# Kernel optimization log

Hardware: AMD Instinct MI355X
Metric: run time of the kernel (lower is better)

Reference implementation:

```python
import jax, jax.numpy as jnp
import numpy as np

B, N, E, H = 16, 512, 512, 8
D = E // H
NEG = -1e9  # stands in for -inf; other scores are clamped to [-10, 10]


def setup_inputs() -> dict:
    key = jax.random.key(0)
    ks = jax.random.split(key, 11)
    s = 1.0 / np.sqrt(E)
    return {
        "x": jax.random.normal(ks[0], (B, N, E), jnp.float32),
        "db": jax.random.normal(ks[1], (B, N, N), jnp.float32),
        "mask": jax.random.randint(ks[2], (B, N), 0, 2, jnp.int32),
        "wq": jax.random.normal(ks[3], (E, E), jnp.float32) * s,
        "bq": jax.random.normal(ks[4], (E,), jnp.float32) * s,
        "wk": jax.random.normal(ks[5], (E, E), jnp.float32) * s,
        "bk": jax.random.normal(ks[6], (E,), jnp.float32) * s,
        "wv": jax.random.normal(ks[7], (E, E), jnp.float32) * s,
        "bv": jax.random.normal(ks[8], (E,), jnp.float32) * s,
        "wo": jax.random.normal(ks[9], (E, E), jnp.float32) * s,
        "bo": jax.random.normal(ks[10], (E,), jnp.float32) * s,
    }


def reference(x, db, mask, wq, bq, wk, bk, wv, bv, wo, bo):
    # projections -> [B, H, N, D]
    def proj(w, b):
        return (x @ w.T + b).reshape(B, N, H, D).transpose(0, 2, 1, 3)

    q = proj(wq, bq)
    k = proj(wk, bk)
    v = proj(wv, bv)

    scale = 1.0 / np.sqrt(D).astype(np.float32)
    sc = jnp.einsum('bhid,bhjd->bhij', q, k) * scale + db[:, None, :, :]
    sc = jnp.clip(sc, -10.0, 10.0)
    sc = jnp.where(mask[:, None, None, :].astype(bool), sc, NEG)
    a = jax.nn.softmax(sc, axis=-1)  # dropout is identity (p=0 / eval)
    o = jnp.einsum('bhij,bhjd->bhid', a, v)
    o = o.transpose(0, 2, 1, 3).reshape(B, N, E)
    return o @ wo.T + bo
```

## Files before the change

### kernel.cpp

```cpp
#include <hip/hip_runtime.h>

typedef __attribute__((ext_vector_type(8))) short short8;
typedef __attribute__((ext_vector_type(4))) short short4v;
typedef __attribute__((ext_vector_type(4))) float f32x4;

#define MFMA16(A, B, C) __builtin_amdgcn_mfma_f32_16x16x32_bf16(A, B, C, 0, 0, 0)

__device__ __forceinline__ short f2bf(float f) {
    union { float f; unsigned u; } v;
    v.f = f;
    unsigned r = (v.u + 0x7FFFu + ((v.u >> 16) & 1u)) >> 16;
    return (short)r;
}

__device__ __forceinline__ float bf2f(short u) {
    union { unsigned u; float f; } v;
    v.u = ((unsigned)(unsigned short)u) << 16;
    return v.f;
}

__global__ __launch_bounds__(256) void cvt_all(
    const float* __restrict__ x, const float* __restrict__ wq,
    const float* __restrict__ wk, const float* __restrict__ wv,
    const float* __restrict__ wo, const float* __restrict__ db,
    const int* __restrict__ mask, short* __restrict__ xb,
    short* __restrict__ wcat, short* __restrict__ wob,
    short* __restrict__ dbp) {
    const int blk = blockIdx.x;
    if (blk < 2560) {
        int i = blk * 256 + threadIdx.x;
        const float* src;
        short* dst;
        int soff, doff;
        if (i < 524288) {
            src = x; dst = xb; soff = i; doff = i;
        } else {
            int j = i - 524288;
            int w = j >> 15;
            soff = j & 32767;
            src = (w == 0) ? wq : (w == 1) ? wk : (w == 2) ? wv : wo;
            if (w < 3) { dst = wcat; doff = j; }
            else       { dst = wob;  doff = soff; }
        }
        const float* p = src + (size_t)soff * 8;
        short8 r;
#pragma unroll
        for (int t = 0; t < 8; ++t) r[t] = f2bf(p[t]);
        *(short8*)(dst + (size_t)doff * 8) = r;
    } else {
        int t = (blk - 2560) * 256 + threadIdx.x;
        int f = t * 8;
        int b = f >> 18;
        int rem = f & 262143;
        int qt = rem >> 13;
        int rem2 = rem & 8191;
        int jidx = rem2 >> 10;
        int w = rem2 & 1023;
        int lane = w >> 4;
        int idx0 = w & 15;
        int c = lane & 15, g = lane >> 4;
        int q = qt * 16 + c;
        const float* dbrow = db + ((size_t)b * 512 + q) * 512;
        const int* mrow = mask + b * 512;
        short8 out;
#pragma unroll
        for (int e = 0; e < 8; ++e) {
            int idx = idx0 + e;
            int nt = idx >> 2, r = idx & 3;
            int j = jidx * 64 + nt * 16 + g * 4 + r;
            float val = (mrow[j] != 0) ? dbrow[j] : -1e9f;
            out[e] = f2bf(val);
        }
        *(short8*)(dbp + (size_t)f) = out;
    }
}

__global__ __launch_bounds__(256) void qkv128(
    const short* __restrict__ A, const short* __restrict__ Bw,
    const float* __restrict__ bq, const float* __restrict__ bk,
    const float* __restrict__ bv, short* __restrict__ qo,
    short* __restrict__ ko, short* __restrict__ vto) {
    __shared__ short As[128 * 72];
    __shared__ short Bs[128 * 72];
    const int tid = threadIdx.x, lane = tid & 63, wid = tid >> 6;
    const int c = lane & 15, g = lane >> 4;
    const int wr = (wid >> 1) * 64, wc = (wid & 1) * 64;
    const int m0 = blockIdx.x * 128, e0 = blockIdx.y * 128;

    const f32x4 Z = {0.f, 0.f, 0.f, 0.f};
    f32x4 acc[4][4];
#pragma unroll
    for (int i = 0; i < 4; ++i)
#pragma unroll
        for (int j = 0; j < 4; ++j) acc[i][j] = Z;

    short8 pa[4], pb[4];
#pragma unroll
    for (int p = 0; p < 4; ++p) {
        int u = p * 256 + tid;
        int row = u >> 3, c8 = u & 7;
        pa[p] = *(const short8*)&A[(size_t)(m0 + row) * 512 + c8 * 8];
        pb[p] = *(const short8*)&Bw[(size_t)(e0 + row) * 512 + c8 * 8];
    }
    for (int it = 0; it < 8; ++it) {
        __syncthreads();
#pragma unroll
        for (int p = 0; p < 4; ++p) {
            int u = p * 256 + tid;
            int row = u >> 3, c8 = u & 7;
            *(short8*)&As[row * 72 + c8 * 8] = pa[p];
            *(short8*)&Bs[row * 72 + c8 * 8] = pb[p];
        }
        if (it < 7) {
            int k0 = (it + 1) * 64;
#pragma unroll
            for (int p = 0; p < 4; ++p) {
                int u = p * 256 + tid;
                int row = u >> 3, c8 = u & 7;
                pa[p] = *(const short8*)&A[(size_t)(m0 + row) * 512 + k0 + c8 * 8];
                pb[p] = *(const short8*)&Bw[(size_t)(e0 + row) * 512 + k0 + c8 * 8];
            }
        }
        __syncthreads();
#pragma unroll
        for (int ks = 0; ks < 2; ++ks) {
            short8 af[4], bf[4];
#pragma unroll
            for (int mt = 0; mt < 4; ++mt)
                af[mt] = *(const short8*)&As[(wr + mt * 16 + c) * 72 + ks * 32 + g * 8];
#pragma unroll
            for (int nt = 0; nt < 4; ++nt)
                bf[nt] = *(const short8*)&Bs[(wc + nt * 16 + c) * 72 + ks * 32 + g * 8];
#pragma unroll
            for (int mt = 0; mt < 4; ++mt)
#pragma unroll
                for (int nt = 0; nt < 4; ++nt)
                    acc[mt][nt] = MFMA16(af[mt], bf[nt], acc[mt][nt]);
        }
    }

    const int z = e0 >> 9;
    const float* bp = (z == 0) ? bq : (z == 1) ? bk : bv;
    if (z < 2) {
        short* out = (z == 0) ? qo : ko;
#pragma unroll
        for (int nt = 0; nt < 4; ++nt) {
            int eh = (e0 & 511) + wc + nt * 16 + c;
            float bsv = bp[eh];
            int h = eh >> 6, d = eh & 63;
#pragma unroll
            for (int mt = 0; mt < 4; ++mt)
#pragma unroll
                for (int r = 0; r < 4; ++r) {
                    int m = m0 + wr + mt * 16 + g * 4 + r;
                    int bb = m >> 9, n = m & 511;
                    out[(((size_t)bb * 8 + h) * 512 + n) * 64 + d] =
                        f2bf(acc[mt][nt][r] + bsv);
                }
        }
    } else {
#pragma unroll
        for (int nt = 0; nt < 4; ++nt) {
            int eh = (e0 & 511) + wc + nt * 16 + c;
            float bsv = bp[eh];
            int h = eh >> 6, d = eh & 63;
#pragma unroll
            for (int mt = 0; mt < 4; ++mt) {
                int m = m0 + wr + mt * 16 + g * 4;
                int bb = m >> 9, n = m & 511;
                short4v w;
#pragma unroll
                for (int r = 0; r < 4; ++r) w[r] = f2bf(acc[mt][nt][r] + bsv);
                *(short4v*)&vto[(((size_t)bb * 8 + h) * 64 + d) * 512 + n] = w;
            }
        }
    }
}

__global__ __launch_bounds__(256) void out128(const short* __restrict__ A,
                                              const short* __restrict__ W,
                                              const float* __restrict__ bo,
                                              float* __restrict__ out) {
    __shared__ short As[128 * 72];
    __shared__ short Bs[128 * 72];
    const int tid = threadIdx.x, lane = tid & 63, wid = tid >> 6;
    const int c = lane & 15, g = lane >> 4;
    const int wr = (wid >> 1) * 64, wc = (wid & 1) * 64;
    const int m0 = blockIdx.x * 128, e0 = blockIdx.y * 128;

    const f32x4 Z = {0.f, 0.f, 0.f, 0.f};
    f32x4 acc[4][4];
#pragma unroll
    for (int i = 0; i < 4; ++i)
#pragma unroll
        for (int j = 0; j < 4; ++j) acc[i][j] = Z;

    short8 pa[4], pb[4];
#pragma unroll
    for (int p = 0; p < 4; ++p) {
        int u = p * 256 + tid;
        int row = u >> 3, c8 = u & 7;
        pa[p] = *(const short8*)&A[(size_t)(m0 + row) * 512 + c8 * 8];
        pb[p] = *(const short8*)&W[(size_t)(e0 + row) * 512 + c8 * 8];
    }
    for (int it = 0; it < 8; ++it) {
        __syncthreads();
#pragma unroll
        for (int p = 0; p < 4; ++p) {
            int u = p * 256 + tid;
            int row = u >> 3, c8 = u & 7;
            *(short8*)&As[row * 72 + c8 * 8] = pa[p];
            *(short8*)&Bs[row * 72 + c8 * 8] = pb[p];
        }
        if (it < 7) {
            int k0 = (it + 1) * 64;
#pragma unroll
            for (int p = 0; p < 4; ++p) {
                int u = p * 256 + tid;
                int row = u >> 3, c8 = u & 7;
                pa[p] = *(const short8*)&A[(size_t)(m0 + row) * 512 + k0 + c8 * 8];
                pb[p] = *(const short8*)&W[(size_t)(e0 + row) * 512 + k0 + c8 * 8];
            }
        }
        __syncthreads();
#pragma unroll
        for (int ks = 0; ks < 2; ++ks) {
            short8 af[4], bf[4];
#pragma unroll
            for (int mt = 0; mt < 4; ++mt)
                af[mt] = *(const short8*)&As[(wr + mt * 16 + c) * 72 + ks * 32 + g * 8];
#pragma unroll
            for (int nt = 0; nt < 4; ++nt)
                bf[nt] = *(const short8*)&Bs[(wc + nt * 16 + c) * 72 + ks * 32 + g * 8];
#pragma unroll
            for (int mt = 0; mt < 4; ++mt)
#pragma unroll
                for (int nt = 0; nt < 4; ++nt)
                    acc[mt][nt] = MFMA16(af[mt], bf[nt], acc[mt][nt]);
        }
    }

#pragma unroll
    for (int nt = 0; nt < 4; ++nt) {
        int e = e0 + wc + nt * 16 + c;
        float bsv = bo[e];
#pragma unroll
        for (int mt = 0; mt < 4; ++mt)
#pragma unroll
            for (int r = 0; r < 4; ++r) {
                int m = m0 + wr + mt * 16 + g * 4 + r;
                out[(size_t)m * 512 + e] = acc[mt][nt][r] + bsv;
            }
    }
}

__global__ __launch_bounds__(256, 2) void attn_mfma(
    const short* __restrict__ q, const short* __restrict__ k,
    const short* __restrict__ vt, const short* __restrict__ dbp_all,
    short* __restrict__ o) {
    __shared__ short pl[8][16 * 72];
    const int tid = threadIdx.x;
    const int lane = tid & 63, wid = tid >> 6;
    const int c = lane & 15, g = lane >> 4;
    const int f = blockIdx.x;
    const int blo = f & 7;
    const int t = f >> 3;
    const int u4 = t & 3;
    const int h = (t >> 2) & 7;
    const int b = (t >> 5) * 8 + blo;
    const int u = u4 * 4 + wid;
    const int q0A = u * 32;

    const short* kp = k + (((size_t)b * 8 + h) * 512) * 64;
    const short* vp = vt + (((size_t)b * 8 + h) * 64) * 512;
    const short* qpA = q + (((size_t)b * 8 + h) * 512 + q0A) * 64;
    const short* dbpA = dbp_all + (((size_t)b * 32 + u * 2) * 8) * 1024 + lane * 16;
    const short* dbpB = dbpA + 8192;

    short8 qA0 = *(const short8*)&qpA[c * 64 + g * 8];
    short8 qA1 = *(const short8*)&qpA[c * 64 + 32 + g * 8];
    short8 qB0 = *(const short8*)&qpA[(16 + c) * 64 + g * 8];
    short8 qB1 = *(const short8*)&qpA[(16 + c) * 64 + 32 + g * 8];

    short8 kf0[4], kf1[4];
#pragma unroll
    for (int nt = 0; nt < 4; ++nt) {
        kf0[nt] = *(const short8*)&kp[(nt * 16 + c) * 64 + g * 8];
        kf1[nt] = *(const short8*)&kp[(nt * 16 + c) * 64 + 32 + g * 8];
    }
    short8 dA0 = *(const short8*)&dbpA[0];
    short8 dA1 = *(const short8*)&dbpA[8];
    short8 dB0 = *(const short8*)&dbpB[0];
    short8 dB1 = *(const short8*)&dbpB[8];

    const f32x4 Z = {0.f, 0.f, 0.f, 0.f};
    f32x4 oA[4], oB[4];
    float lsA[4], lsB[4];
#pragma unroll
    for (int dt = 0; dt < 4; ++dt) { oA[dt] = Z; oB[dt] = Z; }
#pragma unroll
    for (int nt = 0; nt < 4; ++nt) { lsA[nt] = 0.f; lsB[nt] = 0.f; }

    short* plA = &pl[wid * 2][0];
    short* plB = &pl[wid * 2 + 1][0];

    for (int jidx = 0; jidx < 8; ++jidx) {
        const int j0 = jidx * 64;
        f32x4 sA[4], sB[4];
        __builtin_amdgcn_s_setprio(1);
#pragma unroll
        for (int nt = 0; nt < 4; ++nt) {
            f32x4 zA = Z, zB = Z;
            zA = MFMA16(kf0[nt], qA0, zA);
            zB = MFMA16(kf0[nt], qB0, zB);
            zA = MFMA16(kf1[nt], qA1, zA);
            zB = MFMA16(kf1[nt], qB1, zB);
            sA[nt] = zA;
            sB[nt] = zB;
        }
        __builtin_amdgcn_s_setprio(0);
        if (jidx < 7) {
#pragma unroll
            for (int nt = 0; nt < 4; ++nt) {
                kf0[nt] = *(const short8*)&kp[(j0 + 64 + nt * 16 + c) * 64 + g * 8];
                kf1[nt] = *(const short8*)&kp[(j0 + 64 + nt * 16 + c) * 64 + 32 + g * 8];
            }
        }
        short8 vf0[4], vf1[4];
#pragma unroll
        for (int dt = 0; dt < 4; ++dt) {
            vf0[dt] = *(const short8*)&vp[(dt * 16 + c) * 512 + j0 + g * 8];
            vf1[dt] = *(const short8*)&vp[(dt * 16 + c) * 512 + j0 + 32 + g * 8];
        }
#pragma unroll
        for (int nt = 0; nt < 4; ++nt) {
            short4v w;
            float ps0 = 0.f, ps1 = 0.f;
#pragma unroll
            for (int r = 0; r < 4; ++r) {
                int idx = nt * 4 + r;
                float dv = bf2f(idx < 8 ? dA0[idx] : dA1[idx - 8]);
                float v = fminf(fmaxf(fmaf(sA[nt][r], 0.125f, dv), -10.f), 10.f);
                float pp = exp2f(fmaf(v, 1.442695041f, -14.42695041f));
                w[r] = f2bf(pp);
                if (r < 2) ps0 += pp; else ps1 += pp;
            }
            lsA[nt] += ps0 + ps1;
            *(short4v*)&plA[c * 72 + nt * 16 + g * 4] = w;
        }
        if (jidx < 7) {
            dA0 = *(const short8*)&dbpA[(jidx + 1) * 1024];
            dA1 = *(const short8*)&dbpA[(jidx + 1) * 1024 + 8];
        }
#pragma unroll
        for (int nt = 0; nt < 4; ++nt) {
            short4v w;
            float ps0 = 0.f, ps1 = 0.f;
#pragma unroll
            for (int r = 0; r < 4; ++r) {
                int idx = nt * 4 + r;
                float dv = bf2f(idx < 8 ? dB0[idx] : dB1[idx - 8]);
                float v = fminf(fmaxf(fmaf(sB[nt][r], 0.125f, dv), -10.f), 10.f);
                float pp = exp2f(fmaf(v, 1.442695041f, -14.42695041f));
                w[r] = f2bf(pp);
                if (r < 2) ps0 += pp; else ps1 += pp;
            }
            lsB[nt] += ps0 + ps1;
            *(short4v*)&plB[c * 72 + nt * 16 + g * 4] = w;
        }
        if (jidx < 7) {
            dB0 = *(const short8*)&dbpB[(jidx + 1) * 1024];
            dB1 = *(const short8*)&dbpB[(jidx + 1) * 1024 + 8];
        }
        asm volatile("s_waitcnt lgkmcnt(0)" ::: "memory");
        __builtin_amdgcn_sched_barrier(0);
        short8 pA0 = *(const short8*)&plA[c * 72 + g * 8];
        short8 pA1 = *(const short8*)&plA[c * 72 + 32 + g * 8];
        short8 pB0 = *(const short8*)&plB[c * 72 + g * 8];
        short8 pB1 = *(const short8*)&plB[c * 72 + 32 + g * 8];
        __builtin_amdgcn_s_setprio(1);
#pragma unroll
        for (int dt = 0; dt < 4; ++dt) {
            oA[dt] = MFMA16(vf0[dt], pA0, oA[dt]);
            oB[dt] = MFMA16(vf0[dt], pB0, oB[dt]);
            oA[dt] = MFMA16(vf1[dt], pA1, oA[dt]);
            oB[dt] = MFMA16(vf1[dt], pB1, oB[dt]);
        }
        __builtin_amdgcn_s_setprio(0);
    }
    float lA = (lsA[0] + lsA[1]) + (lsA[2] + lsA[3]);
    lA += __shfl_xor(lA, 16);
    lA += __shfl_xor(lA, 32);
    float lB = (lsB[0] + lsB[1]) + (lsB[2] + lsB[3]);
    lB += __shfl_xor(lB, 16);
    lB += __shfl_xor(lB, 32);
    const float invA = 1.f / lA, invB = 1.f / lB;
#pragma unroll
    for (int dt = 0; dt < 4; ++dt) {
        short4v wa, wb;
#pragma unroll
        for (int r = 0; r < 4; ++r) {
            wa[r] = f2bf(oA[dt][r] * invA);
            wb[r] = f2bf(oB[dt][r] * invB);
        }
        *(short4v*)&o[((size_t)b * 512 + q0A + c) * 512 + h * 64 + dt * 16 + g * 4] = wa;
        *(short4v*)&o[((size_t)b * 512 + q0A + 16 + c) * 512 + h * 64 + dt * 16 + g * 4] = wb;
    }
}

extern "C" void kernel_launch(void* const* d_in, const int* in_sizes, int n_in,
                              void* d_out, int out_size, void* d_ws, size_t ws_size,
                              hipStream_t stream) {
    const float* x  = (const float*)d_in[0];
    const float* db = (const float*)d_in[1];
    const int* msk  = (const int*)d_in[2];
    const float* wq = (const float*)d_in[3];
    const float* bq = (const float*)d_in[4];
    const float* wk = (const float*)d_in[5];
    const float* bk = (const float*)d_in[6];
    const float* wv = (const float*)d_in[7];
    const float* bv = (const float*)d_in[8];
    const float* wo = (const float*)d_in[9];
    const float* bo = (const float*)d_in[10];
    float* out = (float*)d_out;

    short* xb   = (short*)d_ws;
    short* wcat = xb + 4194304;
    short* wob  = wcat + 786432;
    short* qb   = wob + 262144;
    short* kb   = qb + 4194304;
    short* vtb  = kb + 4194304;
    short* ob   = vtb + 4194304;
    short* dbp  = ob + 4194304;

    cvt_all<<<4608, 256, 0, stream>>>(x, wq, wk, wv, wo, db, msk,
                                      xb, wcat, wob, dbp);
    qkv128<<<dim3(64, 12), 256, 0, stream>>>(xb, wcat, bq, bk, bv, qb, kb, vtb);
    attn_mfma<<<512, 256, 0, stream>>>(qb, kb, vtb, dbp, ob);
    out128<<<dim3(64, 4), 256, 0, stream>>>(ob, wob, bo, out);
}
```

Measured before the change: 88.00 us.

## Stage K and V tiles through double-buffered LDS shared across waves

Each of the four waves in a block previously loaded its own full copy of the K and V tiles straight from global memory into registers. Now the block loads each 64x64 K and V tile cooperatively once into padded, double-buffered LDS, prefetching the next tile into registers and storing it after the PV MFMAs. Waves then read their MFMA fragments from LDS. This cuts global/L2 traffic by the wave count, in exchange for extra LDS traffic, a block-wide barrier per iteration, and more shared memory that may affect occupancy.

```diff
diff --git a/kernel.cpp b/kernel.cpp
--- a/kernel.cpp
+++ b/kernel.cpp
@@ -258,6 +258,8 @@
     const short* __restrict__ q, const short* __restrict__ k,
     const short* __restrict__ vt, const short* __restrict__ dbp_all,
     short* __restrict__ o) {
+    __shared__ short Ks[2][64 * 72];
+    __shared__ short Vs[2][64 * 72];
     __shared__ short pl[8][16 * 72];
     const int tid = threadIdx.x;
     const int lane = tid & 63, wid = tid >> 6;
@@ -277,21 +279,30 @@
     const short* dbpA = dbp_all + (((size_t)b * 32 + u * 2) * 8) * 1024 + lane * 16;
     const short* dbpB = dbpA + 8192;
 
+    const int s0 = tid * 2, s1 = tid * 2 + 1;
+    const int kr0 = s0 >> 3, kc0 = (s0 & 7) * 8;
+    const int kr1 = s1 >> 3, kc1 = (s1 & 7) * 8;
+
     short8 qA0 = *(const short8*)&qpA[c * 64 + g * 8];
     short8 qA1 = *(const short8*)&qpA[c * 64 + 32 + g * 8];
     short8 qB0 = *(const short8*)&qpA[(16 + c) * 64 + g * 8];
     short8 qB1 = *(const short8*)&qpA[(16 + c) * 64 + 32 + g * 8];
 
-    short8 kf0[4], kf1[4];
-#pragma unroll
-    for (int nt = 0; nt < 4; ++nt) {
-        kf0[nt] = *(const short8*)&kp[(nt * 16 + c) * 64 + g * 8];
-        kf1[nt] = *(const short8*)&kp[(nt * 16 + c) * 64 + 32 + g * 8];
+    {
+        short8 k0v = *(const short8*)&kp[kr0 * 64 + kc0];
+        short8 k1v = *(const short8*)&kp[kr1 * 64 + kc1];
+        short8 v0v = *(const short8*)&vp[kr0 * 512 + kc0];
+        short8 v1v = *(const short8*)&vp[kr1 * 512 + kc1];
+        *(short8*)&Ks[0][kr0 * 72 + kc0] = k0v;
+        *(short8*)&Ks[0][kr1 * 72 + kc1] = k1v;
+        *(short8*)&Vs[0][kr0 * 72 + kc0] = v0v;
+        *(short8*)&Vs[0][kr1 * 72 + kc1] = v1v;
     }
     short8 dA0 = *(const short8*)&dbpA[0];
     short8 dA1 = *(const short8*)&dbpA[8];
     short8 dB0 = *(const short8*)&dbpB[0];
     short8 dB1 = *(const short8*)&dbpB[8];
+    __syncthreads();
 
     const f32x4 Z = {0.f, 0.f, 0.f, 0.f};
     f32x4 oA[4], oB[4];
@@ -305,32 +316,31 @@
     short* plB = &pl[wid * 2 + 1][0];
 
     for (int jidx = 0; jidx < 8; ++jidx) {
+        const int cur = jidx & 1;
         const int j0 = jidx * 64;
+        short8 kn0, kn1, vn0, vn1;
+        if (jidx < 7) {
+            const int jn = j0 + 64;
+            kn0 = *(const short8*)&kp[(jn + kr0) * 64 + kc0];
+            kn1 = *(const short8*)&kp[(jn + kr1) * 64 + kc1];
+            vn0 = *(const short8*)&vp[kr0 * 512 + jn + kc0];
+            vn1 = *(const short8*)&vp[kr1 * 512 + jn + kc1];
+        }
+        short8 kf0, kf1;
         f32x4 sA[4], sB[4];
-        __builtin_amdgcn_s_setprio(1);
 #pragma unroll
         for (int nt = 0; nt < 4; ++nt) {
+            kf0 = *(const short8*)&Ks[cur][(nt * 16 + c) * 72 + g * 8];
+            kf1 = *(const short8*)&Ks[cur][(nt * 16 + c) * 72 + 32 + g * 8];
             f32x4 zA = Z, zB = Z;
-            zA = MFMA16(kf0[nt], qA0, zA);
-            zB = MFMA16(kf0[nt], qB0, zB);
-            zA = MFMA16(kf1[nt], qA1, zA);
-            zB = MFMA16(kf1[nt], qB1, zB);
+            __builtin_amdgcn_s_setprio(1);
+            zA = MFMA16(kf0, qA0, zA);
+            zB = MFMA16(kf0, qB0, zB);
+            zA = MFMA16(kf1, qA1, zA);
+            zB = MFMA16(kf1, qB1, zB);
+            __builtin_amdgcn_s_setprio(0);
             sA[nt] = zA;
             sB[nt] = zB;
-        }
-        __builtin_amdgcn_s_setprio(0);
-        if (jidx < 7) {
-#pragma unroll
-            for (int nt = 0; nt < 4; ++nt) {
-                kf0[nt] = *(const short8*)&kp[(j0 + 64 + nt * 16 + c) * 64 + g * 8];
-                kf1[nt] = *(const short8*)&kp[(j0 + 64 + nt * 16 + c) * 64 + 32 + g * 8];
-            }
-        }
-        short8 vf0[4], vf1[4];
-#pragma unroll
-        for (int dt = 0; dt < 4; ++dt) {
-            vf0[dt] = *(const short8*)&vp[(dt * 16 + c) * 512 + j0 + g * 8];
-            vf1[dt] = *(const short8*)&vp[(dt * 16 + c) * 512 + j0 + 32 + g * 8];
         }
 #pragma unroll
         for (int nt = 0; nt < 4; ++nt) {
@@ -378,15 +388,25 @@
         short8 pA1 = *(const short8*)&plA[c * 72 + 32 + g * 8];
         short8 pB0 = *(const short8*)&plB[c * 72 + g * 8];
         short8 pB1 = *(const short8*)&plB[c * 72 + 32 + g * 8];
-        __builtin_amdgcn_s_setprio(1);
 #pragma unroll
         for (int dt = 0; dt < 4; ++dt) {
-            oA[dt] = MFMA16(vf0[dt], pA0, oA[dt]);
-            oB[dt] = MFMA16(vf0[dt], pB0, oB[dt]);
-            oA[dt] = MFMA16(vf1[dt], pA1, oA[dt]);
-            oB[dt] = MFMA16(vf1[dt], pB1, oB[dt]);
-        }
-        __builtin_amdgcn_s_setprio(0);
+            short8 vf0 = *(const short8*)&Vs[cur][(dt * 16 + c) * 72 + g * 8];
+            short8 vf1 = *(const short8*)&Vs[cur][(dt * 16 + c) * 72 + 32 + g * 8];
+            __builtin_amdgcn_s_setprio(1);
+            oA[dt] = MFMA16(vf0, pA0, oA[dt]);
+            oB[dt] = MFMA16(vf0, pB0, oB[dt]);
+            oA[dt] = MFMA16(vf1, pA1, oA[dt]);
+            oB[dt] = MFMA16(vf1, pB1, oB[dt]);
+            __builtin_amdgcn_s_setprio(0);
+        }
+        if (jidx < 7) {
+            const int nxt = cur ^ 1;
+            *(short8*)&Ks[nxt][kr0 * 72 + kc0] = kn0;
+            *(short8*)&Ks[nxt][kr1 * 72 + kc1] = kn1;
+            *(short8*)&Vs[nxt][kr0 * 72 + kc0] = vn0;
+            *(short8*)&Vs[nxt][kr1 * 72 + kc1] = vn1;
+            __syncthreads();
+        }
     }
     float lA = (lsA[0] + lsA[1]) + (lsA[2] + lsA[3]);
     lA += __shfl_xor(lA, 16);
```

Result: faster. 76.32 us (-13.3%).
